# Optimization experiments

Hardware: AMD Instinct MI355X
Metric: run time of the kernel (lower is better)

The kernel has to match this reference:

```python
import jax, jax.numpy as jnp
import numpy as np

N = 50000   # nodes
E = 800000  # edges
F_IN, F_HID, F_OUT = 128, 96, 40


def setup_inputs() -> dict:
    key = jax.random.key(0)
    ks = jax.random.split(key, 9)
    x = jax.random.normal(ks[0], (N, F_IN), dtype=jnp.float32)
    edge_index = jax.random.randint(ks[1], (2, E), 0, N, dtype=jnp.int32)
    def lin(k, fi, fo):
        s = 1.0 / np.sqrt(fi)
        return jax.random.uniform(k, (fi, fo), jnp.float32, -s, s)
    W1 = lin(ks[2], F_IN, F_HID)
    b1 = jnp.zeros((F_HID,), jnp.float32)
    W2 = lin(ks[3], F_HID, F_HID)
    b2 = jnp.zeros((F_HID,), jnp.float32)
    Wout = lin(ks[4], F_HID, F_OUT)
    bout = jnp.zeros((F_OUT,), jnp.float32)
    return {"x": x, "edge_index": edge_index, "W1": W1, "b1": b1,
            "W2": W2, "b2": b2, "Wout": Wout, "bout": bout}


def _gcn_norm(edge_index, n):
    # add self-loops, symmetric degree normalization (PyG GCNConv default)
    loops = jnp.arange(n, dtype=edge_index.dtype)
    src = jnp.concatenate([edge_index[0], loops])
    dst = jnp.concatenate([edge_index[1], loops])
    deg = jax.ops.segment_sum(jnp.ones_like(dst, dtype=jnp.float32), dst,
                              num_segments=n)
    dinv = jnp.where(deg > 0, jax.lax.rsqrt(deg), 0.0)
    norm = dinv[src] * dinv[dst]   # [E+N]
    return src, dst, norm


def _gcn_layer(h, src, dst, norm, W, b, n):
    # linear transform, then normalized scatter-add aggregation, then bias
    h = h @ W                                 # [N, Fout]
    msg = h[src] * norm[:, None]              # gather + scale
    agg = jax.ops.segment_sum(msg, dst, num_segments=n)
    return agg + b


def reference(x, edge_index, W1, b1, W2, b2, Wout, bout):
    n = x.shape[0]
    src, dst, norm = _gcn_norm(edge_index, n)
    h = jax.nn.relu(_gcn_layer(x, src, dst, norm, W1, b1, n))
    h = jax.nn.relu(_gcn_layer(h, src, dst, norm, W2, b2, n))
    return h @ Wout + bout
```

## Files before the change

kernel.cpp:

```cpp
#include <hip/hip_runtime.h>
#include <hip/hip_fp16.h>

#define N_NODES 50000
#define N_EDGES 800000
#define F_INN   128
#define F_HID   96
#define F_OUTT  40


__global__ void count_kernel(const int* __restrict__ dst, int* __restrict__ counts,
                             int* __restrict__ rank, int e) {
    int i = blockIdx.x * blockDim.x + threadIdx.x;
    if (i < e) rank[i] = atomicAdd(&counts[dst[i]], 1);
}

__global__ __launch_bounds__(1024) void scan_local_kernel(
        const int* __restrict__ counts, int* __restrict__ row_start,
        float* __restrict__ dinv, int* __restrict__ blk_sums, int n) {
    __shared__ int wave_sums[16];
    int tid = threadIdx.x, lane = tid & 63, wid = tid >> 6;
    int i = blockIdx.x * 1024 + tid;
    int v = (i < n) ? counts[i] : 0;
    int val = v;
    #pragma unroll
    for (int off = 1; off < 64; off <<= 1) {
        int u = __shfl_up(val, off, 64);
        if (lane >= off) val += u;
    }
    if (lane == 63) wave_sums[wid] = val;
    __syncthreads();
    if (wid == 0) {
        int w = (lane < 16) ? wave_sums[lane] : 0;
        #pragma unroll
        for (int off = 1; off < 16; off <<= 1) {
            int u = __shfl_up(w, off, 64);
            if (lane >= off) w += u;
        }
        if (lane < 16) wave_sums[lane] = w;
    }
    __syncthreads();
    int excl = ((wid == 0) ? 0 : wave_sums[wid - 1]) + (val - v);
    if (i < n) {
        row_start[i] = excl;
        dinv[i] = rsqrtf((float)(v + 1));
    }
    if (tid == 0) blk_sums[blockIdx.x] = wave_sums[15];
}

__global__ void scan_blk_kernel(const int* __restrict__ blk_sums, int* __restrict__ blk_off,
                                int* __restrict__ row_start, int n, int nblk) {
    int lane = threadIdx.x;
    int v = (lane < nblk) ? blk_sums[lane] : 0;
    int val = v;
    #pragma unroll
    for (int off = 1; off < 64; off <<= 1) {
        int u = __shfl_up(val, off, 64);
        if (lane >= off) val += u;
    }
    if (lane < nblk) blk_off[lane] = val - v;
    if (lane == 63) row_start[n] = val;
}

__global__ __launch_bounds__(1024) void scan_apply_kernel(
        int* __restrict__ row_start, const int* __restrict__ blk_off, int n) {
    int i = blockIdx.x * 1024 + threadIdx.x;
    if (i < n) row_start[i] += blk_off[blockIdx.x];
}

__global__ void fill_csr_kernel(const int* __restrict__ src, const int* __restrict__ dst,
                                const int* __restrict__ rank, const int* __restrict__ row_start,
                                int* __restrict__ csr_src, int e) {
    int i = blockIdx.x * blockDim.x + threadIdx.x;
    if (i >= e) return;
    csr_src[row_start[dst[i]] + rank[i]] = src[i];
}


template <int FI>
__global__ __launch_bounds__(384) void gemm96_kernel(
        const float* __restrict__ A, const float* __restrict__ W,
        const float* __restrict__ dinv, __half2* __restrict__ C, int n) {
    __shared__ float Wlds[FI * 96];
    int tid = threadIdx.y * 24 + threadIdx.x;
    for (int i = tid; i < FI * 24; i += 384)
        reinterpret_cast<float4*>(Wlds)[i] = reinterpret_cast<const float4*>(W)[i];
    __syncthreads();

    int j  = threadIdx.x * 4;
    int n0 = blockIdx.x * 64 + threadIdx.y;
    int nn[4];
    #pragma unroll
    for (int t = 0; t < 4; ++t) nn[t] = min(n0 + 16 * t, n - 1);

    float4 acc[4];
    #pragma unroll
    for (int t = 0; t < 4; ++t) acc[t] = make_float4(0.f, 0.f, 0.f, 0.f);

    for (int k = 0; k < FI; k += 4) {
        float4 a[4];
        #pragma unroll
        for (int t = 0; t < 4; ++t)
            a[t] = *reinterpret_cast<const float4*>(A + (size_t)nn[t] * FI + k);
        float4 w0 = *reinterpret_cast<const float4*>(Wlds + (k + 0) * 96 + j);
        float4 w1 = *reinterpret_cast<const float4*>(Wlds + (k + 1) * 96 + j);
        float4 w2 = *reinterpret_cast<const float4*>(Wlds + (k + 2) * 96 + j);
        float4 w3 = *reinterpret_cast<const float4*>(Wlds + (k + 3) * 96 + j);
        #pragma unroll
        for (int t = 0; t < 4; ++t) {
            acc[t].x += a[t].x * w0.x + a[t].y * w1.x + a[t].z * w2.x + a[t].w * w3.x;
            acc[t].y += a[t].x * w0.y + a[t].y * w1.y + a[t].z * w2.y + a[t].w * w3.y;
            acc[t].z += a[t].x * w0.z + a[t].y * w1.z + a[t].z * w2.z + a[t].w * w3.z;
            acc[t].w += a[t].x * w0.w + a[t].y * w1.w + a[t].z * w2.w + a[t].w * w3.w;
        }
    }
    #pragma unroll
    for (int t = 0; t < 4; ++t) {
        int node = n0 + 16 * t;
        if (node < n) {
            float dn = dinv[node];
            __half2 h01 = __floats2half2_rn(acc[t].x * dn, acc[t].y * dn);
            __half2 h23 = __floats2half2_rn(acc[t].z * dn, acc[t].w * dn);
            __half2* Cp = C + (size_t)node * 48 + (j >> 1);
            Cp[0] = h01;
            Cp[1] = h23;
        }
    }
}

__global__ __launch_bounds__(320) void gemm_out_kernel(
        const float* __restrict__ A, const float* __restrict__ W,
        const float* __restrict__ bias, float* __restrict__ C, int n) {
    __shared__ float Wlds[96 * 40];
    int tid = threadIdx.y * 10 + threadIdx.x;
    for (int i = tid; i < 96 * 10; i += 320)
        reinterpret_cast<float4*>(Wlds)[i] = reinterpret_cast<const float4*>(W)[i];
    __syncthreads();

    int j    = threadIdx.x * 4;
    int node = blockIdx.x * 32 + threadIdx.y;
    int nc   = min(node, n - 1);
    float4 acc = make_float4(0.f, 0.f, 0.f, 0.f);
    for (int k = 0; k < 96; k += 4) {
        float4 a = *reinterpret_cast<const float4*>(A + (size_t)nc * 96 + k);
        float4 w0 = *reinterpret_cast<const float4*>(Wlds + (k + 0) * 40 + j);
        float4 w1 = *reinterpret_cast<const float4*>(Wlds + (k + 1) * 40 + j);
        float4 w2 = *reinterpret_cast<const float4*>(Wlds + (k + 2) * 40 + j);
        float4 w3 = *reinterpret_cast<const float4*>(Wlds + (k + 3) * 40 + j);
        acc.x += a.x * w0.x + a.y * w1.x + a.z * w2.x + a.w * w3.x;
        acc.y += a.x * w0.y + a.y * w1.y + a.z * w2.y + a.w * w3.y;
        acc.z += a.x * w0.z + a.y * w1.z + a.z * w2.z + a.w * w3.z;
        acc.w += a.x * w0.w + a.y * w1.w + a.z * w2.w + a.w * w3.w;
    }
    if (node < n) {
        float4 b = *reinterpret_cast<const float4*>(bias + j);
        acc.x += b.x; acc.y += b.y; acc.z += b.z; acc.w += b.w;
        *reinterpret_cast<float4*>(C + (size_t)node * 40 + j) = acc;
    }
}


__global__ __launch_bounds__(256) void agg_kernel(
        const __half2* __restrict__ T, const int* __restrict__ row_start,
        const int* __restrict__ csr_src, const float* __restrict__ dinv,
        const float* __restrict__ bias, float* __restrict__ H, int n) {
    int lane = threadIdx.x & 63;
    int node = __builtin_amdgcn_readfirstlane(blockIdx.x * 4 + (threadIdx.x >> 6));
    if (node >= n) return;
    int fl = min(lane, 47);

    float2 self = __half22float2(T[(size_t)node * 48 + fl]);
    float accx = self.x, accy = self.y;

    int idx = row_start[node];
    int end = row_start[node + 1];
    for (; idx + 4 <= end; idx += 4) {
        int s0 = csr_src[idx + 0];
        int s1 = csr_src[idx + 1];
        int s2 = csr_src[idx + 2];
        int s3 = csr_src[idx + 3];
        __half2 a0 = T[(size_t)s0 * 48 + fl];
        __half2 a1 = T[(size_t)s1 * 48 + fl];
        __half2 a2 = T[(size_t)s2 * 48 + fl];
        __half2 a3 = T[(size_t)s3 * 48 + fl];
        float2 f0 = __half22float2(a0);
        float2 f1 = __half22float2(a1);
        float2 f2 = __half22float2(a2);
        float2 f3 = __half22float2(a3);
        accx += f0.x + f1.x + f2.x + f3.x;
        accy += f0.y + f1.y + f2.y + f3.y;
    }
    for (; idx < end; ++idx) {
        float2 f = __half22float2(T[(size_t)csr_src[idx] * 48 + fl]);
        accx += f.x; accy += f.y;
    }
    if (lane < 48) {
        float dn = dinv[node];
        float2 b = reinterpret_cast<const float2*>(bias)[lane];
        float2 o;
        o.x = fmaxf(dn * accx + b.x, 0.f);
        o.y = fmaxf(dn * accy + b.y, 0.f);
        reinterpret_cast<float2*>(H)[(size_t)node * 48 + lane] = o;
    }
}


extern "C" void kernel_launch(void* const* d_in, const int* in_sizes, int n_in,
                              void* d_out, int out_size, void* d_ws, size_t ws_size,
                              hipStream_t stream) {
    const float* x    = (const float*)d_in[0];
    const int*   ei   = (const int*)d_in[1];
    const float* W1   = (const float*)d_in[2];
    const float* b1   = (const float*)d_in[3];
    const float* W2   = (const float*)d_in[4];
    const float* b2   = (const float*)d_in[5];
    const float* Wout = (const float*)d_in[6];
    const float* bout = (const float*)d_in[7];
    float*       out  = (float*)d_out;

    const int* src = ei;
    const int* dst = ei + N_EDGES;

    char* ws = (char*)d_ws;
    size_t off = 0;
    auto alloc = [&](size_t bytes) {
        size_t o = off;
        off = (off + bytes + 511) & ~(size_t)511;
        return (void*)(ws + o);
    };
    int*     counts    = (int*)    alloc(N_NODES * sizeof(int));
    int*     row_start = (int*)    alloc((N_NODES + 1) * sizeof(int));
    float*   dinv      = (float*)  alloc(N_NODES * sizeof(float));
    int*     blk_sums  = (int*)    alloc(64 * sizeof(int));
    int*     blk_off   = (int*)    alloc(64 * sizeof(int));
    int*     rank      = (int*)    alloc((size_t)N_EDGES * sizeof(int));
    int*     csr_src   = (int*)    alloc((size_t)N_EDGES * sizeof(int));
    __half2* Th        = (__half2*)alloc((size_t)N_NODES * 48 * sizeof(__half2));
    float*   Hf        = (float*)  alloc((size_t)N_NODES * F_HID * sizeof(float));

    const int NSCAN = (N_NODES + 1023) / 1024;

    hipMemsetAsync(counts, 0, N_NODES * sizeof(int), stream);
    count_kernel<<<(N_EDGES + 255) / 256, 256, 0, stream>>>(dst, counts, rank, N_EDGES);
    scan_local_kernel<<<NSCAN, 1024, 0, stream>>>(counts, row_start, dinv, blk_sums, N_NODES);
    scan_blk_kernel<<<1, 64, 0, stream>>>(blk_sums, blk_off, row_start, N_NODES, NSCAN);
    scan_apply_kernel<<<NSCAN, 1024, 0, stream>>>(row_start, blk_off, N_NODES);
    fill_csr_kernel<<<(N_EDGES + 255) / 256, 256, 0, stream>>>(
        src, dst, rank, row_start, csr_src, N_EDGES);

    gemm96_kernel<F_INN><<<(N_NODES + 63) / 64, dim3(24, 16), 0, stream>>>(
        x, W1, dinv, Th, N_NODES);
    agg_kernel<<<(N_NODES + 3) / 4, 256, 0, stream>>>(
        Th, row_start, csr_src, dinv, b1, Hf, N_NODES);

    gemm96_kernel<F_HID><<<(N_NODES + 63) / 64, dim3(24, 16), 0, stream>>>(
        Hf, W2, dinv, Th, N_NODES);
    agg_kernel<<<(N_NODES + 3) / 4, 256, 0, stream>>>(
        Th, row_start, csr_src, dinv, b2, Hf, N_NODES);

    gemm_out_kernel<<<(N_NODES + 31) / 32, dim3(10, 32), 0, stream>>>(
        Hf, Wout, bout, out, N_NODES);
}
```

Before: 271.7 us.

## Split each wavefront across five edges with 16-byte gathers in aggregation

The aggregation kernel now gives each 64-lane wavefront five groups of 12 lanes. Each group handles a different incoming edge and each lane loads 8 half-precision features as one float4. The next source index is prefetched one iteration ahead, and partial sums are combined across groups with shuffles before the bias, ReLU and vectorised store. This aims to raise memory-level parallelism and cut per-edge instruction count on the gather-bound step, at the cost of 4 idle lanes and a 40-shuffle reduction per node.

After: 279.8 us. 1.03x slower.

```diff
diff --git a/kernel.cpp b/kernel.cpp
--- a/kernel.cpp
+++ b/kernel.cpp
@@ -159,47 +159,76 @@
 }
 
 
+__device__ inline void acc8(float* acc, float4 r) {
+    const __half2* h = reinterpret_cast<const __half2*>(&r);
+    #pragma unroll
+    for (int i = 0; i < 4; ++i) {
+        float2 f2 = __half22float2(h[i]);
+        acc[2 * i]     += f2.x;
+        acc[2 * i + 1] += f2.y;
+    }
+}
+
 __global__ __launch_bounds__(256) void agg_kernel(
-        const __half2* __restrict__ T, const int* __restrict__ row_start,
-        const int* __restrict__ csr_src, const float* __restrict__ dinv,
-        const float* __restrict__ bias, float* __restrict__ H, int n) {
+        const float4* __restrict__ T4,
+        const int* __restrict__ row_start,
+        const int* __restrict__ csr_src,
+        const float* __restrict__ dinv,
+        const float* __restrict__ bias,
+        float4* __restrict__ H4, int n) {
     int lane = threadIdx.x & 63;
     int node = __builtin_amdgcn_readfirstlane(blockIdx.x * 4 + (threadIdx.x >> 6));
     if (node >= n) return;
-    int fl = min(lane, 47);
-
-    float2 self = __half22float2(T[(size_t)node * 48 + fl]);
-    float accx = self.x, accy = self.y;
-
-    int idx = row_start[node];
+    int e = lane / 12;
+    int f = lane - e * 12;
+    bool lact = (e < 5);
+
+    float acc[8];
+    #pragma unroll
+    for (int i = 0; i < 8; ++i) acc[i] = 0.f;
+
+    if (e == 0) acc8(acc, T4[(size_t)node * 12 + f]);
+
+    int beg = row_start[node];
     int end = row_start[node + 1];
-    for (; idx + 4 <= end; idx += 4) {
-        int s0 = csr_src[idx + 0];
-        int s1 = csr_src[idx + 1];
-        int s2 = csr_src[idx + 2];
-        int s3 = csr_src[idx + 3];
-        __half2 a0 = T[(size_t)s0 * 48 + fl];
-        __half2 a1 = T[(size_t)s1 * 48 + fl];
-        __half2 a2 = T[(size_t)s2 * 48 + fl];
-        __half2 a3 = T[(size_t)s3 * 48 + fl];
-        float2 f0 = __half22float2(a0);
-        float2 f1 = __half22float2(a1);
-        float2 f2 = __half22float2(a2);
-        float2 f3 = __half22float2(a3);
-        accx += f0.x + f1.x + f2.x + f3.x;
-        accy += f0.y + f1.y + f2.y + f3.y;
-    }
-    for (; idx < end; ++idx) {
-        float2 f = __half22float2(T[(size_t)csr_src[idx] * 48 + fl]);
-        accx += f.x; accy += f.y;
-    }
-    if (lane < 48) {
+
+    int p = beg + e;
+    bool v = lact && (p < end);
+    int s = v ? csr_src[p] : node;
+    for (int idx = beg; idx < end; idx += 5) {
+        int  pn = p + 5;
+        bool vn = lact && (pn < end);
+        int  sn = vn ? csr_src[pn] : node;
+        float4 r = T4[(size_t)s * 12 + f];
+        if (v) acc8(acc, r);
+        p = pn; v = vn; s = sn;
+    }
+
+    float tot[8];
+    #pragma unroll
+    for (int i = 0; i < 8; ++i) tot[i] = acc[i];
+    #pragma unroll
+    for (int k = 1; k < 5; ++k) {
+        #pragma unroll
+        for (int i = 0; i < 8; ++i)
+            tot[i] += __shfl(acc[i], f + 12 * k, 64);
+    }
+
+    if (e == 0) {
         float dn = dinv[node];
-        float2 b = reinterpret_cast<const float2*>(bias)[lane];
-        float2 o;
-        o.x = fmaxf(dn * accx + b.x, 0.f);
-        o.y = fmaxf(dn * accy + b.y, 0.f);
-        reinterpret_cast<float2*>(H)[(size_t)node * 48 + lane] = o;
+        const float4* b4 = reinterpret_cast<const float4*>(bias);
+        float4 b0 = b4[2 * f], b1 = b4[2 * f + 1];
+        float4 o0, o1;
+        o0.x = fmaxf(dn * tot[0] + b0.x, 0.f);
+        o0.y = fmaxf(dn * tot[1] + b0.y, 0.f);
+        o0.z = fmaxf(dn * tot[2] + b0.z, 0.f);
+        o0.w = fmaxf(dn * tot[3] + b0.w, 0.f);
+        o1.x = fmaxf(dn * tot[4] + b1.x, 0.f);
+        o1.y = fmaxf(dn * tot[5] + b1.y, 0.f);
+        o1.z = fmaxf(dn * tot[6] + b1.z, 0.f);
+        o1.w = fmaxf(dn * tot[7] + b1.w, 0.f);
+        H4[(size_t)node * 24 + 2 * f]     = o0;
+        H4[(size_t)node * 24 + 2 * f + 1] = o1;
     }
 }
 
@@ -250,12 +279,12 @@
     gemm96_kernel<F_INN><<<(N_NODES + 63) / 64, dim3(24, 16), 0, stream>>>(
         x, W1, dinv, Th, N_NODES);
     agg_kernel<<<(N_NODES + 3) / 4, 256, 0, stream>>>(
-        Th, row_start, csr_src, dinv, b1, Hf, N_NODES);
+        (const float4*)Th, row_start, csr_src, dinv, b1, (float4*)Hf, N_NODES);
 
     gemm96_kernel<F_HID><<<(N_NODES + 63) / 64, dim3(24, 16), 0, stream>>>(
         Hf, W2, dinv, Th, N_NODES);
     agg_kernel<<<(N_NODES + 3) / 4, 256, 0, stream>>>(
-        Th, row_start, csr_src, dinv, b2, Hf, N_NODES);
+        (const float4*)Th, row_start, csr_src, dinv, b2, (float4*)Hf, N_NODES);
 
     gemm_out_kernel<<<(N_NODES + 31) / 32, dim3(10, 32), 0, stream>>>(
         Hf, Wout, bout, out, N_NODES);
```
